# Performance work log

Measured on AMD Instinct MI355X. Metric: run time of the kernel, lower is better.

Reference implementation:

```python
import jax, jax.numpy as jnp
import numpy as np

S, B, D = 2048, 2, 4096
H, KVH, HD = 32, 8, 128          # n_heads_q, n_kv_heads, head_dim
NREP = H // KVH                  # GQA repeat factor
ROPE_BASE = 10000.0


def _rope(x, cos, sin):
    # x: [B, S, h, HD]; cos/sin: [S, HD//2]
    xr = x.reshape(x.shape[:-1] + (-1, 2))
    x0, x1 = xr[..., 0], xr[..., 1]
    c = cos[None, :, None, :]
    s = sin[None, :, None, :]
    out = jnp.stack([x0 * c - x1 * s, x0 * s + x1 * c], axis=-1)
    return out.reshape(x.shape)


def setup_inputs() -> dict:
    key = jax.random.key(0)
    k0, k1, k2, k3, k4 = jax.random.split(key, 5)
    x = jax.random.normal(k0, (S, B, D), jnp.float32)
    inv_freq = 1.0 / (ROPE_BASE ** (np.arange(0, HD, 2, dtype=np.float64) / HD))  # [HD//2]
    t = np.arange(S, dtype=np.float64)[:, None] * inv_freq[None, :]               # [S, HD//2]
    freqs_cos = jnp.asarray(np.cos(t), jnp.float32)
    freqs_sin = jnp.asarray(np.sin(t), jnp.float32)
    scale = 0.02
    wq = jax.random.normal(k1, (H * HD, D), jnp.float32) * scale
    wk = jax.random.normal(k2, (KVH * HD, D), jnp.float32) * scale
    wv = jax.random.normal(k3, (KVH * HD, D), jnp.float32) * scale
    wo = jax.random.normal(k4, (D, H * HD), jnp.float32) * scale
    return {"x": x, "start_pos": 0, "freqs_cos": freqs_cos, "freqs_sin": freqs_sin,
            "wq": wq, "wk": wk, "wv": wv, "wo": wo}


def reference(x, start_pos, freqs_cos, freqs_sin, wq, wk, wv, wo):
    seq_len, batch, _ = x.shape
    # QKV projections (torch Linear: y = x @ W^T), then [S,B,*] -> [B,S,h,HD]
    q = (x @ wq.T).transpose(1, 0, 2).reshape(batch, seq_len, H, HD)
    k = (x @ wk.T).transpose(1, 0, 2).reshape(batch, seq_len, KVH, HD)
    v = (x @ wv.T).transpose(1, 0, 2).reshape(batch, seq_len, KVH, HD)
    # RoPE on q and k
    q = _rope(q, freqs_cos, freqs_sin)
    k = _rope(k, freqs_cos, freqs_sin)
    # repeat_kv (GQA)
    k = jnp.repeat(k, NREP, axis=2)
    v = jnp.repeat(v, NREP, axis=2)
    # [B, H, S, HD]
    q = q.transpose(0, 2, 1, 3)
    k = k.transpose(0, 2, 1, 3)
    v = v.transpose(0, 2, 1, 3)
    # causal scaled dot-product attention (SDPA is_causal=True equivalent)
    scores = jnp.einsum('bhqd,bhkd->bhqk', q, k) / np.float32(np.sqrt(HD))
    causal = jnp.tril(jnp.ones((seq_len, seq_len), dtype=bool))
    scores = jnp.where(causal[None, None], scores, jnp.float32(-jnp.inf))
    probs = jax.nn.softmax(scores.astype(jnp.float32), axis=-1).astype(q.dtype)
    out = jnp.einsum('bhqk,bhkd->bhqd', probs, v)
    # [B,H,S,HD] -> [B,S,H*HD] -> [S,B,H*HD]
    out = out.transpose(0, 2, 1, 3).reshape(batch, seq_len, H * HD).transpose(1, 0, 2)
    return out @ wo.T
```

## Files before the change

kernel.cpp:

```cpp
#include <hip/hip_runtime.h>

typedef __attribute__((ext_vector_type(8))) short s16x8;
typedef __attribute__((ext_vector_type(8))) __bf16 bf16x8;
typedef __attribute__((ext_vector_type(4))) float f32x4;

#define S_LEN 2048
#define KDIM  4096
#define CSOFT 0.12751743f

__device__ __forceinline__ unsigned short f2bf(float f) {
  unsigned u = __builtin_bit_cast(unsigned, f);
  u += 0x7fffu + ((u >> 16) & 1u);
  return (unsigned short)(u >> 16);
}

__device__ __forceinline__ f32x4 mfma_bf16(s16x8 a, s16x8 b, f32x4 c) {
  return __builtin_amdgcn_mfma_f32_16x16x32_bf16(
      __builtin_bit_cast(bf16x8, a), __builtin_bit_cast(bf16x8, b), c, 0, 0, 0);
}

__device__ __forceinline__ void gload_lds16(const unsigned short* g, void* l) {
  __builtin_amdgcn_global_load_lds(
      (const __attribute__((address_space(1))) void*)g,
      (__attribute__((address_space(3))) void*)l, 16, 0, 0);
}

__global__ void cvt_bf16(const float* __restrict__ in,
                         unsigned short* __restrict__ out, int n8) {
  int i = blockIdx.x * 256 + threadIdx.x;
  if (i >= n8) return;
  const float* p = in + (size_t)i * 8;
  f32x4 a = *(const f32x4*)(p);
  f32x4 b = *(const f32x4*)(p + 4);
  s16x8 v;
  v[0] = (short)f2bf(a[0]); v[1] = (short)f2bf(a[1]);
  v[2] = (short)f2bf(a[2]); v[3] = (short)f2bf(a[3]);
  v[4] = (short)f2bf(b[0]); v[5] = (short)f2bf(b[1]);
  v[6] = (short)f2bf(b[2]); v[7] = (short)f2bf(b[3]);
  *(s16x8*)(out + (size_t)i * 8) = v;
}

template <int EPI, int N, bool B_FP32>
__global__ __launch_bounds__(256, 2)
void gemm_bt(const unsigned short* __restrict__ A,
             const float* __restrict__ Bw32,
             const unsigned short* __restrict__ Bw16,
             void* __restrict__ Out,
             const float* __restrict__ cosT,
             const float* __restrict__ sinT) {
  const int K = KDIM;
  const int tid = threadIdx.x;
  const int lane = tid & 63, wid = tid >> 6;
  const int l15 = lane & 15, l4 = lane >> 4;
  const int nct = N / 128;
  const int ct = blockIdx.x % nct, rt = blockIdx.x / nct;
  const int row0 = rt * 128, col0 = ct * 128;
  const int wr = wid >> 1, wc = wid & 1;

  __shared__ __align__(16) unsigned short As[128 * 32];
  __shared__ __align__(16) unsigned short Bs[128 * 32];

  f32x4 acc[4][4];
#pragma unroll
  for (int i = 0; i < 4; i++)
#pragma unroll
    for (int j = 0; j < 4; j++) acc[i][j] = f32x4{0.f, 0.f, 0.f, 0.f};

  for (int kt = 0; kt < K; kt += 32) {
#pragma unroll
    for (int i = 0; i < 2; i++) {
      int j = wid * 2 + i;
      int ch = j * 64 + lane;
      int r = ch >> 2, c = ch & 3;
      int sc = c ^ ((r >> 1) & 3);
      gload_lds16(A + (size_t)(row0 + r) * K + kt + sc * 8, (char*)As + j * 1024);
    }
    if (B_FP32) {
#pragma unroll
      for (int j = 0; j < 2; j++) {
        int ch = tid + 256 * j;
        int r = ch >> 2, c = ch & 3;
        const float* src = Bw32 + (size_t)(col0 + r) * K + kt + c * 8;
        f32x4 f0 = *(const f32x4*)(src);
        f32x4 f1 = *(const f32x4*)(src + 4);
        s16x8 v;
        v[0] = (short)f2bf(f0[0]); v[1] = (short)f2bf(f0[1]);
        v[2] = (short)f2bf(f0[2]); v[3] = (short)f2bf(f0[3]);
        v[4] = (short)f2bf(f1[0]); v[5] = (short)f2bf(f1[1]);
        v[6] = (short)f2bf(f1[2]); v[7] = (short)f2bf(f1[3]);
        int sw = c ^ ((r >> 1) & 3);
        *(s16x8*)((char*)Bs + r * 64 + sw * 16) = v;
      }
    } else {
#pragma unroll
      for (int i = 0; i < 2; i++) {
        int j = wid * 2 + i;
        int ch = j * 64 + lane;
        int r = ch >> 2, c = ch & 3;
        int sc = c ^ ((r >> 1) & 3);
        gload_lds16(Bw16 + (size_t)(col0 + r) * K + kt + sc * 8, (char*)Bs + j * 1024);
      }
    }
    __syncthreads();

    s16x8 af[4], bfr[4];
#pragma unroll
    for (int mi = 0; mi < 4; mi++) {
      int r = wr * 64 + mi * 16 + l15;
      int sw = l4 ^ ((r >> 1) & 3);
      af[mi] = *(const s16x8*)((char*)As + r * 64 + sw * 16);
    }
#pragma unroll
    for (int ni = 0; ni < 4; ni++) {
      int r = wc * 64 + ni * 16 + l15;
      int sw = l4 ^ ((r >> 1) & 3);
      bfr[ni] = *(const s16x8*)((char*)Bs + r * 64 + sw * 16);
    }
#pragma unroll
    for (int mi = 0; mi < 4; mi++)
#pragma unroll
      for (int ni = 0; ni < 4; ni++)
        acc[mi][ni] = mfma_bf16(af[mi], bfr[ni], acc[mi][ni]);
    __syncthreads();
  }

#pragma unroll
  for (int mi = 0; mi < 4; mi++) {
#pragma unroll
    for (int ni = 0; ni < 4; ni++) {
      f32x4 v = acc[mi][ni];
      int rowb = row0 + wr * 64 + mi * 16 + l4 * 4;
      int col = col0 + wc * 64 + ni * 16 + l15;
      if (EPI == 3) {
        float* o = (float*)Out;
#pragma unroll
        for (int r = 0; r < 4; r++) o[(size_t)(rowb + r) * 4096 + col] = v[r];
      } else {
        if (EPI != 2) {
          float vp[4];
#pragma unroll
          for (int r = 0; r < 4; r++) vp[r] = __shfl_xor(v[r], 1, 64);
          bool odd = lane & 1;
          int fi = (col & 127) >> 1;
#pragma unroll
          for (int r = 0; r < 4; r++) {
            int n = rowb + r, s = n >> 1;
            float c = cosT[s * 64 + fi], sn = sinT[s * 64 + fi];
            v[r] = odd ? (vp[r] * sn + v[r] * c) : (v[r] * c - vp[r] * sn);
          }
        }
        unsigned short* o = (unsigned short*)Out;
        int hh = col >> 7, hd = col & 127;
#pragma unroll
        for (int r = 0; r < 4; r++) {
          int n = rowb + r, s = n >> 1, b = n & 1;
          size_t idx;
          if (EPI == 0)      idx = ((size_t)(b * 32 + hh) * 2048 + s) * 128 + hd;
          else if (EPI == 1) idx = ((size_t)(b * 8 + hh) * 2048 + s) * 128 + hd;
          else               idx = ((size_t)(b * 8 + hh) * 128 + hd) * 2048 + s;
          o[idx] = f2bf(v[r]);
        }
      }
    }
  }
}

__global__ __launch_bounds__(256, 2)
void attn_fwd(const unsigned short* __restrict__ Qa,
              const unsigned short* __restrict__ Ka,
              const unsigned short* __restrict__ Vt,
              unsigned short* __restrict__ AO) {
  int bid = blockIdx.x;
  int pid = bid & 7;
  int h = (bid >> 3) & 31;
  int b = bid >> 8;
  int kvh = h >> 2;
  int tid = threadIdx.x, lane = tid & 63, wid = tid >> 6;
  int l15 = lane & 15, l4 = lane >> 4;

  __shared__ __align__(16) unsigned short Ks[64 * 128];
  __shared__ __align__(16) unsigned short Vs[128 * 64];
  __shared__ __align__(16) unsigned short Ps[4][32 * 64];

  const unsigned short* Qp = Qa + ((size_t)(b * 32 + h) * 2048) * 128;
  const unsigned short* Kp = Ka + ((size_t)(b * 8 + kvh) * 2048) * 128;
  const unsigned short* Vp = Vt + ((size_t)(b * 8 + kvh) * 128) * 2048;

  for (int half = 0; half < 2; half++) {
    int qt = half == 0 ? (7 - pid) : (8 + pid);
    int q0 = qt * 128, qr0 = q0 + wid * 32;

    s16x8 qf[2][4];
#pragma unroll
    for (int mi = 0; mi < 2; mi++)
#pragma unroll
      for (int ks = 0; ks < 4; ks++)
        qf[mi][ks] = *(const s16x8*)(Qp + (size_t)(qr0 + mi * 16 + l15) * 128 +
                                     ks * 32 + l4 * 8);

    f32x4 o[2][8];
#pragma unroll
    for (int mi = 0; mi < 2; mi++)
#pragma unroll
      for (int nb = 0; nb < 8; nb++) o[mi][nb] = f32x4{0.f, 0.f, 0.f, 0.f};
    float m[2][4], lsum[2][4];
#pragma unroll
    for (int mi = 0; mi < 2; mi++)
#pragma unroll
      for (int pr = 0; pr < 4; pr++) { m[mi][pr] = -1e30f; lsum[mi][pr] = 0.f; }

    int nt = q0 / 64 + 2;
    for (int t = 0; t < nt; t++) {
      int s0 = t * 64;
      const unsigned short* ktp = Kp + (size_t)s0 * 128;
#pragma unroll
      for (int i = 0; i < 4; i++) {
        int j = wid * 4 + i;
        int ch = j * 64 + lane;
        {
          int r = ch >> 4, cl = ch & 15;
          int sc = (cl & 8) | ((cl ^ (r & 7)) & 7);
          gload_lds16(ktp + r * 128 + sc * 8, (char*)Ks + j * 1024);
        }
        {
          int r = ch >> 3, p = ch & 7;
          int sc = p ^ (r & 7);
          gload_lds16(Vp + (size_t)r * 2048 + s0 + sc * 8, (char*)Vs + j * 1024);
        }
      }
      __syncthreads();

      if (s0 <= qr0 + 31) {
        f32x4 sc[2][4];
#pragma unroll
        for (int mi = 0; mi < 2; mi++)
#pragma unroll
          for (int kb = 0; kb < 4; kb++) sc[mi][kb] = f32x4{0.f, 0.f, 0.f, 0.f};
#pragma unroll
        for (int kb = 0; kb < 4; kb++) {
          int r = kb * 16 + l15;
#pragma unroll
          for (int ks = 0; ks < 4; ks++) {
            int c = ks * 4 + l4;
            int sw = (c & 8) | ((c ^ (r & 7)) & 7);
            s16x8 kf = *(const s16x8*)((char*)Ks + r * 256 + sw * 16);
            sc[0][kb] = mfma_bf16(qf[0][ks], kf, sc[0][kb]);
            sc[1][kb] = mfma_bf16(qf[1][ks], kf, sc[1][kb]);
          }
        }
        bool needmask = (s0 + 63) > qr0;
#pragma unroll
        for (int mi = 0; mi < 2; mi++) {
          if (needmask) {
#pragma unroll
            for (int kb = 0; kb < 4; kb++) {
              int kg = s0 + kb * 16 + l15;
#pragma unroll
              for (int pr = 0; pr < 4; pr++) {
                int qg = qr0 + mi * 16 + l4 * 4 + pr;
                if (kg > qg) sc[mi][kb][pr] = -1e30f;
              }
            }
          }
          float rm[4];
#pragma unroll
          for (int pr = 0; pr < 4; pr++)
            rm[pr] = fmaxf(fmaxf(sc[mi][0][pr], sc[mi][1][pr]),
                           fmaxf(sc[mi][2][pr], sc[mi][3][pr]));
#pragma unroll
          for (int xm = 1; xm <= 8; xm <<= 1)
#pragma unroll
            for (int pr = 0; pr < 4; pr++)
              rm[pr] = fmaxf(rm[pr], __shfl_xor(rm[pr], xm, 64));
          bool grow = false;
#pragma unroll
          for (int pr = 0; pr < 4; pr++)
            grow = grow || ((rm[pr] - m[mi][pr]) * CSOFT > 8.f);
          if (__any(grow)) {
            float fac[4];
#pragma unroll
            for (int pr = 0; pr < 4; pr++) {
              float nm = fmaxf(m[mi][pr], rm[pr]);
              fac[pr] = __builtin_amdgcn_exp2f((m[mi][pr] - nm) * CSOFT);
              m[mi][pr] = nm;
              lsum[mi][pr] *= fac[pr];
            }
#pragma unroll
            for (int nb = 0; nb < 8; nb++)
#pragma unroll
              for (int pr = 0; pr < 4; pr++) o[mi][nb][pr] *= fac[pr];
          }
          float rs[4] = {0.f, 0.f, 0.f, 0.f};
#pragma unroll
          for (int kb = 0; kb < 4; kb++)
#pragma unroll
            for (int pr = 0; pr < 4; pr++) {
              float p = __builtin_amdgcn_exp2f((sc[mi][kb][pr] - m[mi][pr]) * CSOFT);
              sc[mi][kb][pr] = p;
              rs[pr] += p;
            }
#pragma unroll
          for (int xm = 1; xm <= 8; xm <<= 1)
#pragma unroll
            for (int pr = 0; pr < 4; pr++) rs[pr] += __shfl_xor(rs[pr], xm, 64);
#pragma unroll
          for (int pr = 0; pr < 4; pr++) lsum[mi][pr] += rs[pr];
          char* pb = (char*)(&Ps[wid][0]);
#pragma unroll
          for (int kb = 0; kb < 4; kb++) {
            int col = kb * 16 + l15;
#pragma unroll
            for (int pr = 0; pr < 4; pr++) {
              int row = mi * 16 + l4 * 4 + pr;
              *(unsigned short*)(pb + row * 128 + (((col >> 3) ^ (row & 7)) * 16) +
                                 (col & 7) * 2) = f2bf(sc[mi][kb][pr]);
            }
          }
        }
        char* pb = (char*)(&Ps[wid][0]);
#pragma unroll
        for (int ks = 0; ks < 2; ks++) {
          s16x8 pa[2];
#pragma unroll
          for (int mi = 0; mi < 2; mi++) {
            int row = mi * 16 + l15;
            int c = ks * 4 + l4;
            pa[mi] = *(const s16x8*)(pb + row * 128 + ((c ^ (row & 7)) * 16));
          }
#pragma unroll
          for (int nb = 0; nb < 8; nb++) {
            int r = nb * 16 + l15;
            int c = ks * 4 + l4;
            s16x8 vf = *(const s16x8*)((char*)Vs + r * 128 + ((c ^ (r & 7)) * 16));
            o[0][nb] = mfma_bf16(pa[0], vf, o[0][nb]);
            o[1][nb] = mfma_bf16(pa[1], vf, o[1][nb]);
          }
        }
      }
      __syncthreads();
    }

#pragma unroll
    for (int mi = 0; mi < 2; mi++) {
      float inv[4];
#pragma unroll
      for (int pr = 0; pr < 4; pr++) inv[pr] = 1.f / lsum[mi][pr];
#pragma unroll
      for (int nb = 0; nb < 8; nb++) {
        int col = h * 128 + nb * 16 + l15;
#pragma unroll
        for (int pr = 0; pr < 4; pr++) {
          int q = qr0 + mi * 16 + l4 * 4 + pr;
          AO[(size_t)(q * 2 + b) * 4096 + col] = f2bf(o[mi][nb][pr] * inv[pr]);
        }
      }
    }
  }
}

extern "C" void kernel_launch(void* const* d_in, const int* in_sizes, int n_in,
                              void* d_out, int out_size, void* d_ws, size_t ws_size,
                              hipStream_t stream) {
  const float* x = (const float*)d_in[0];
  const float* cosT = (const float*)d_in[2];
  const float* sinT = (const float*)d_in[3];
  const float* wq = (const float*)d_in[4];
  const float* wk = (const float*)d_in[5];
  const float* wv = (const float*)d_in[6];
  const float* wo = (const float*)d_in[7];
  float* out = (float*)d_out;

  char* ws = (char*)d_ws;
  unsigned short* xb = (unsigned short*)(ws);
  unsigned short* Qa = (unsigned short*)(ws + 33554432ull);
  unsigned short* Ka = (unsigned short*)(ws + 67108864ull);
  unsigned short* Vt = (unsigned short*)(ws + 75497472ull);
  unsigned short* AO = (unsigned short*)(ws + 83886080ull);
  unsigned short* wqb = (unsigned short*)(ws + 117440512ull);
  unsigned short* wkb = (unsigned short*)(ws + 150994944ull);
  unsigned short* wvb = (unsigned short*)(ws + 159383552ull);
  unsigned short* wob = (unsigned short*)(ws + 167772160ull);
  bool wcvt = ws_size >= 201326592ull;

  cvt_bf16<<<8192, 256, 0, stream>>>(x, xb, 2097152);
  if (wcvt) {
    cvt_bf16<<<8192, 256, 0, stream>>>(wq, wqb, 2097152);
    cvt_bf16<<<2048, 256, 0, stream>>>(wk, wkb, 524288);
    cvt_bf16<<<2048, 256, 0, stream>>>(wv, wvb, 524288);
    cvt_bf16<<<8192, 256, 0, stream>>>(wo, wob, 2097152);
    gemm_bt<0, 4096, false><<<1024, 256, 0, stream>>>(xb, nullptr, wqb, Qa, cosT, sinT);
    gemm_bt<1, 1024, false><<<256, 256, 0, stream>>>(xb, nullptr, wkb, Ka, cosT, sinT);
    gemm_bt<2, 1024, false><<<256, 256, 0, stream>>>(xb, nullptr, wvb, Vt, cosT, sinT);
  } else {
    gemm_bt<0, 4096, true><<<1024, 256, 0, stream>>>(xb, wq, nullptr, Qa, cosT, sinT);
    gemm_bt<1, 1024, true><<<256, 256, 0, stream>>>(xb, wk, nullptr, Ka, cosT, sinT);
    gemm_bt<2, 1024, true><<<256, 256, 0, stream>>>(xb, wv, nullptr, Vt, cosT, sinT);
  }
  attn_fwd<<<512, 256, 0, stream>>>(Qa, Ka, Vt, AO);
  if (wcvt) {
    gemm_bt<3, 4096, false><<<1024, 256, 0, stream>>>(AO, nullptr, wob, out, cosT, sinT);
  } else {
    gemm_bt<3, 4096, true><<<1024, 256, 0, stream>>>(AO, wo, nullptr, out, cosT, sinT);
  }
}
```

Baseline: 670.3 us.

## Add 256x256-tile bf16 GEMM with staged async LDS prefetch for Q and O projections

Adds a gemm256 kernel using 256x256 output tiles with 8 waves. It double-buffers LDS through direct global-to-LDS loads, interleaved with MFMA phases, and uses XOR-swizzled LDS addressing, s_setprio and a remapped block order for L2 locality. The Q projection (with its fused RoPE epilogue) and the output projection move to this kernel; the K and V projections keep the old 128-tile GEMM. The larger tiles aim to raise arithmetic intensity and hide load latency. In exchange, the grid shrinks to 256 blocks with heavy register pressure, and the many barriers per k-step can stall waves.

```diff
diff --git a/kernel.cpp b/kernel.cpp
--- a/kernel.cpp
+++ b/kernel.cpp
@@ -38,6 +38,171 @@
   v[4] = (short)f2bf(b[0]); v[5] = (short)f2bf(b[1]);
   v[6] = (short)f2bf(b[2]); v[7] = (short)f2bf(b[3]);
   *(s16x8*)(out + (size_t)i * 8) = v;
+}
+
+template <int EPI>
+__global__ __launch_bounds__(512, 2)
+void gemm256(const unsigned short* __restrict__ A,
+             const unsigned short* __restrict__ B,
+             void* __restrict__ Out,
+             const float* __restrict__ cosT,
+             const float* __restrict__ sinT) {
+  const int K = KDIM;
+  const int NT = KDIM / 32;
+  __shared__ __align__(16) unsigned short As[2][256 * 32];
+  __shared__ __align__(16) unsigned short Bs[2][256 * 32];
+
+  const int tid = threadIdx.x;
+  const int lane = tid & 63, wid = tid >> 6;
+  const int l15 = lane & 15, l4 = lane >> 4;
+  const int wc = wid;
+
+  int bid = blockIdx.x;
+  int wg = (bid & 7) * 32 + (bid >> 3);
+  const int rt = wg >> 4, ct = wg & 15;
+  const int row0 = rt * 256, col0 = ct * 256;
+
+  {}
+  const int ch = wid * 64 + lane;
+  const int sL = ch >> 3, ss = ch & 7;
+  const int su = ss ^ (sL & 7);
+  const int sr = 2 * sL + (su >> 2);
+  const int sc = (su & 3) * 8;
+  const unsigned short* Asrc = A + (size_t)(row0 + sr) * K + sc;
+  const unsigned short* Bsrc = B + (size_t)(col0 + sr) * K + sc;
+
+  const int rdoff = (l15 >> 1) * 128 +
+                    (((((l15 & 1) << 2) | l4) ^ ((l15 >> 1) & 7)) << 4);
+
+  f32x4 acc[16][2];
+#pragma unroll
+  for (int i = 0; i < 16; i++) {
+    acc[i][0] = f32x4{0.f, 0.f, 0.f, 0.f};
+    acc[i][1] = f32x4{0.f, 0.f, 0.f, 0.f};
+  }
+
+  auto stage = [&](int buf, int half, bool isB, int kt) {
+    const unsigned short* src =
+        (isB ? Bsrc : Asrc) + (size_t)half * 128 * K + kt;
+    char* dst = (char*)(isB ? &Bs[buf][0] : &As[buf][0]) + half * 8192 +
+                wid * 1024;
+    gload_lds16(src, dst);
+  };
+
+  stage(0, 0, true, 0);
+  stage(0, 1, true, 0);
+  stage(0, 0, false, 0);
+  stage(0, 1, false, 0);
+  asm volatile("s_waitcnt vmcnt(1)" ::: "memory");
+  __builtin_amdgcn_s_barrier();
+  __builtin_amdgcn_sched_barrier(0);
+
+  for (int t = 0; t < NT; ++t) {
+    const int cur = t & 1, nxt = cur ^ 1;
+    const int ktn = (t + 1) * 32;
+    const bool pf = (t + 1) < NT;
+    const char* Ab = (const char*)&As[cur][0];
+    const char* Bb = (const char*)&Bs[cur][0];
+
+    s16x8 bf0 = *(const s16x8*)(Bb + wc * 2048 + rdoff);
+    s16x8 bf1 = *(const s16x8*)(Bb + wc * 2048 + 1024 + rdoff);
+    s16x8 afA[8];
+#pragma unroll
+    for (int mi = 0; mi < 8; mi++)
+      afA[mi] = *(const s16x8*)(Ab + mi * 1024 + rdoff);
+    if (pf) stage(nxt, 0, true, ktn);
+    __builtin_amdgcn_s_barrier();
+    __builtin_amdgcn_sched_barrier(0);
+    __builtin_amdgcn_s_setprio(1);
+#pragma unroll
+    for (int mi = 0; mi < 4; mi++) {
+      acc[mi][0] = mfma_bf16(afA[mi], bf0, acc[mi][0]);
+      acc[mi][1] = mfma_bf16(afA[mi], bf1, acc[mi][1]);
+    }
+    __builtin_amdgcn_s_setprio(0);
+    if (pf) { asm volatile("s_waitcnt vmcnt(1)" ::: "memory"); }
+    else    { asm volatile("s_waitcnt vmcnt(0)" ::: "memory"); }
+    __builtin_amdgcn_s_barrier();
+    __builtin_amdgcn_sched_barrier(0);
+
+    s16x8 afB[8];
+#pragma unroll
+    for (int mi = 0; mi < 8; mi++)
+      afB[mi] = *(const s16x8*)(Ab + 8192 + mi * 1024 + rdoff);
+    if (pf) stage(nxt, 1, true, ktn);
+    __builtin_amdgcn_s_barrier();
+    __builtin_amdgcn_sched_barrier(0);
+    __builtin_amdgcn_s_setprio(1);
+#pragma unroll
+    for (int mi = 4; mi < 8; mi++) {
+      acc[mi][0] = mfma_bf16(afA[mi], bf0, acc[mi][0]);
+      acc[mi][1] = mfma_bf16(afA[mi], bf1, acc[mi][1]);
+    }
+    __builtin_amdgcn_s_setprio(0);
+    __builtin_amdgcn_s_barrier();
+    __builtin_amdgcn_sched_barrier(0);
+
+    if (pf) stage(nxt, 0, false, ktn);
+    __builtin_amdgcn_s_barrier();
+    __builtin_amdgcn_sched_barrier(0);
+    __builtin_amdgcn_s_setprio(1);
+#pragma unroll
+    for (int mi = 0; mi < 4; mi++) {
+      acc[8 + mi][0] = mfma_bf16(afB[mi], bf0, acc[8 + mi][0]);
+      acc[8 + mi][1] = mfma_bf16(afB[mi], bf1, acc[8 + mi][1]);
+    }
+    __builtin_amdgcn_s_setprio(0);
+    __builtin_amdgcn_s_barrier();
+    __builtin_amdgcn_sched_barrier(0);
+
+    if (pf) stage(nxt, 1, false, ktn);
+    __builtin_amdgcn_s_barrier();
+    __builtin_amdgcn_sched_barrier(0);
+    __builtin_amdgcn_s_setprio(1);
+#pragma unroll
+    for (int mi = 4; mi < 8; mi++) {
+      acc[8 + mi][0] = mfma_bf16(afB[mi], bf0, acc[8 + mi][0]);
+      acc[8 + mi][1] = mfma_bf16(afB[mi], bf1, acc[8 + mi][1]);
+    }
+    __builtin_amdgcn_s_setprio(0);
+    if (pf) { asm volatile("s_waitcnt vmcnt(1)" ::: "memory"); }
+    __builtin_amdgcn_s_barrier();
+    __builtin_amdgcn_sched_barrier(0);
+  }
+
+#pragma unroll
+  for (int mi = 0; mi < 16; mi++) {
+#pragma unroll
+    for (int ni = 0; ni < 2; ni++) {
+      f32x4 v = acc[mi][ni];
+      int rowb = row0 + mi * 16 + l4 * 4;
+      int col = col0 + wc * 32 + ni * 16 + l15;
+      if (EPI == 3) {
+        float* o = (float*)Out;
+#pragma unroll
+        for (int r = 0; r < 4; r++) o[(size_t)(rowb + r) * 4096 + col] = v[r];
+      } else {
+        float vp[4];
+#pragma unroll
+        for (int r = 0; r < 4; r++) vp[r] = __shfl_xor(v[r], 1, 64);
+        bool odd = lane & 1;
+        int fi = (col & 127) >> 1;
+#pragma unroll
+        for (int r = 0; r < 4; r++) {
+          int n = rowb + r, s = n >> 1;
+          float c = cosT[s * 64 + fi], sn = sinT[s * 64 + fi];
+          v[r] = odd ? (vp[r] * sn + v[r] * c) : (v[r] * c - vp[r] * sn);
+        }
+        unsigned short* o = (unsigned short*)Out;
+        int hh = col >> 7, hd = col & 127;
+#pragma unroll
+        for (int r = 0; r < 4; r++) {
+          int n = rowb + r, s = n >> 1, b = n & 1;
+          o[((size_t)(b * 32 + hh) * 2048 + s) * 128 + hd] = f2bf(v[r]);
+        }
+      }
+    }
+  }
 }
 
 template <int EPI, int N, bool B_FP32>
@@ -388,7 +553,7 @@
     cvt_bf16<<<2048, 256, 0, stream>>>(wk, wkb, 524288);
     cvt_bf16<<<2048, 256, 0, stream>>>(wv, wvb, 524288);
     cvt_bf16<<<8192, 256, 0, stream>>>(wo, wob, 2097152);
-    gemm_bt<0, 4096, false><<<1024, 256, 0, stream>>>(xb, nullptr, wqb, Qa, cosT, sinT);
+    gemm256<0><<<256, 512, 0, stream>>>(xb, wqb, Qa, cosT, sinT);
     gemm_bt<1, 1024, false><<<256, 256, 0, stream>>>(xb, nullptr, wkb, Ka, cosT, sinT);
     gemm_bt<2, 1024, false><<<256, 256, 0, stream>>>(xb, nullptr, wvb, Vt, cosT, sinT);
   } else {
@@ -398,7 +563,7 @@
   }
   attn_fwd<<<512, 256, 0, stream>>>(Qa, Ka, Vt, AO);
   if (wcvt) {
-    gemm_bt<3, 4096, false><<<1024, 256, 0, stream>>>(AO, nullptr, wob, out, cosT, sinT);
+    gemm256<3><<<256, 512, 0, stream>>>(AO, wob, out, cosT, sinT);
   } else {
     gemm_bt<3, 4096, true><<<1024, 256, 0, stream>>>(AO, wo, nullptr, out, cosT, sinT);
   }
```

New measurement: 640.9 us. 4.4% less time.

## Add 256x256-tile 8-wave GEMM with interleaved LDS staging for Q and O projections

Applied to the files above, without the earlier changes.

Introduces a new GEMM kernel with 256x256 output tiles, 512 threads, double-buffered LDS staged via global_load_lds, XOR-swizzled LDS layout, sub-phase interleaving of loads and MFMAs with setprio, and an XCD-aware block remap. It replaces the 128x128 GEMM for the Q projection (with RoPE epilogue) and the output projection when bf16 weights are available. Larger tiles halve global traffic per FLOP. The cost is one block per CU with heavy register use, and only 256 blocks, which may underfill a GPU with 256 CUs.

```diff
diff --git a/kernel.cpp b/kernel.cpp
--- a/kernel.cpp
+++ b/kernel.cpp
@@ -38,6 +38,194 @@
   v[4] = (short)f2bf(b[0]); v[5] = (short)f2bf(b[1]);
   v[6] = (short)f2bf(b[2]); v[7] = (short)f2bf(b[3]);
   *(s16x8*)(out + (size_t)i * 8) = v;
+}
+
+template <int EPI>
+__global__ __launch_bounds__(512, 1)
+void gemm256(const unsigned short* __restrict__ A,
+             const unsigned short* __restrict__ B,
+             void* __restrict__ Out,
+             const float* __restrict__ cosT,
+             const float* __restrict__ sinT) {
+  const int K = KDIM;
+  __shared__ __align__(16) unsigned short As[2 * 2 * 8192];
+  __shared__ __align__(16) unsigned short Bs[2 * 2 * 8192];
+
+  const int tid = threadIdx.x;
+  const int lane = tid & 63, wid = tid >> 6;
+  const int l15 = lane & 15, l4 = lane >> 4;
+  const int wr = wid >> 2, wc = wid & 3;
+
+  int bid = blockIdx.x;
+  int wg = (bid & 7) * 32 + (bid >> 3);
+  const int rt = wg >> 4, ct = wg & 15;
+  const int row0 = rt * 256, col0 = ct * 256;
+
+  const int ch0 = tid, ch1 = 512 + tid;
+  const int sr0 = ch0 >> 3, u0 = (ch0 & 7) ^ (sr0 & 7);
+  const int sr1 = ch1 >> 3, u1 = (ch1 & 7) ^ (sr1 & 7);
+  const unsigned short* A0p = A + (size_t)(row0 + sr0) * K + u0 * 8;
+  const unsigned short* A1p = A + (size_t)(row0 + sr1) * K + u1 * 8;
+  const unsigned short* B0p = B + (size_t)(col0 + sr0) * K + u0 * 8;
+  const unsigned short* B1p = B + (size_t)(col0 + sr1) * K + u1 * 8;
+
+  const int rdo0 = l15 * 128 + ((l4 ^ (l15 & 7)) << 4);
+  const int rdo1 = l15 * 128 + (((4 | l4) ^ (l15 & 7)) << 4);
+
+  f32x4 acc[8][4];
+#pragma unroll
+  for (int m = 0; m < 8; m++)
+#pragma unroll
+    for (int n = 0; n < 4; n++) acc[m][n] = f32x4{0.f, 0.f, 0.f, 0.f};
+
+  auto stageA = [&](int buf, int h, int kt) {
+    char* d = (char*)As + buf * 32768 + h * 16384 + wid * 1024;
+    size_t so = (size_t)h * 128 * K + kt;
+    gload_lds16(A0p + so, d);
+    gload_lds16(A1p + so, d + 8192);
+  };
+  auto stageB = [&](int buf, int h, int kt) {
+    char* d = (char*)Bs + buf * 32768 + h * 16384 + wid * 1024;
+    size_t so = (size_t)h * 128 * K + kt;
+    gload_lds16(B0p + so, d);
+    gload_lds16(B1p + so, d + 8192);
+  };
+  auto barsb = [&]() {
+    __builtin_amdgcn_s_barrier();
+    __builtin_amdgcn_sched_barrier(0);
+  };
+
+  stageA(0, 0, 0);
+  stageA(0, 1, 0);
+  stageB(0, 0, 0);
+  stageB(0, 1, 0);
+  stageA(1, 0, 64);
+  asm volatile("s_waitcnt vmcnt(2)" ::: "memory");
+  barsb();
+
+  auto do_tile = [&](int tau, bool s123, bool s4, int vmend) {
+    const int buf = tau & 1;
+    const char* Ab = (const char*)As + buf * 32768 + wr * 16384;
+    const char* Bb = (const char*)Bs + buf * 32768 + (wc >> 1) * 16384 +
+                     (wc & 1) * 8192;
+    const int kt1 = (tau + 1) * 64, kt2 = (tau + 2) * 64;
+    s16x8 af0[4], af1[4], bA0[2], bA1[2], bB0[2], bB1[2];
+
+#pragma unroll
+    for (int mi = 0; mi < 4; mi++) {
+      af0[mi] = *(const s16x8*)(Ab + mi * 2048 + rdo0);
+      af1[mi] = *(const s16x8*)(Ab + mi * 2048 + rdo1);
+    }
+#pragma unroll
+    for (int ni = 0; ni < 2; ni++) {
+      bA0[ni] = *(const s16x8*)(Bb + ni * 2048 + rdo0);
+      bA1[ni] = *(const s16x8*)(Bb + ni * 2048 + rdo1);
+    }
+    if (s123) stageA(buf ^ 1, 1, kt1);
+    barsb();
+    __builtin_amdgcn_s_setprio(1);
+#pragma unroll
+    for (int mi = 0; mi < 4; mi++)
+#pragma unroll
+      for (int ni = 0; ni < 2; ni++) {
+        acc[mi][ni] = mfma_bf16(af0[mi], bA0[ni], acc[mi][ni]);
+        acc[mi][ni] = mfma_bf16(af1[mi], bA1[ni], acc[mi][ni]);
+      }
+    __builtin_amdgcn_s_setprio(0);
+    barsb();
+
+#pragma unroll
+    for (int ni = 0; ni < 2; ni++) {
+      bB0[ni] = *(const s16x8*)(Bb + (2 + ni) * 2048 + rdo0);
+      bB1[ni] = *(const s16x8*)(Bb + (2 + ni) * 2048 + rdo1);
+    }
+    if (s123) stageB(buf ^ 1, 0, kt1);
+    barsb();
+    __builtin_amdgcn_s_setprio(1);
+#pragma unroll
+    for (int mi = 0; mi < 4; mi++)
+#pragma unroll
+      for (int ni = 0; ni < 2; ni++) {
+        acc[mi][2 + ni] = mfma_bf16(af0[mi], bB0[ni], acc[mi][2 + ni]);
+        acc[mi][2 + ni] = mfma_bf16(af1[mi], bB1[ni], acc[mi][2 + ni]);
+      }
+    __builtin_amdgcn_s_setprio(0);
+    barsb();
+
+#pragma unroll
+    for (int mi = 0; mi < 4; mi++) {
+      af0[mi] = *(const s16x8*)(Ab + 8192 + mi * 2048 + rdo0);
+      af1[mi] = *(const s16x8*)(Ab + 8192 + mi * 2048 + rdo1);
+    }
+    if (s123) stageB(buf ^ 1, 1, kt1);
+    barsb();
+    __builtin_amdgcn_s_setprio(1);
+#pragma unroll
+    for (int mi = 0; mi < 4; mi++)
+#pragma unroll
+      for (int ni = 0; ni < 2; ni++) {
+        acc[4 + mi][2 + ni] = mfma_bf16(af0[mi], bB0[ni], acc[4 + mi][2 + ni]);
+        acc[4 + mi][2 + ni] = mfma_bf16(af1[mi], bB1[ni], acc[4 + mi][2 + ni]);
+      }
+    __builtin_amdgcn_s_setprio(0);
+    barsb();
+
+    if (s4) stageA(buf, 0, kt2);
+    barsb();
+    __builtin_amdgcn_s_setprio(1);
+#pragma unroll
+    for (int mi = 0; mi < 4; mi++)
+#pragma unroll
+      for (int ni = 0; ni < 2; ni++) {
+        acc[4 + mi][ni] = mfma_bf16(af0[mi], bA0[ni], acc[4 + mi][ni]);
+        acc[4 + mi][ni] = mfma_bf16(af1[mi], bA1[ni], acc[4 + mi][ni]);
+      }
+    __builtin_amdgcn_s_setprio(0);
+    if (vmend == 2) {
+      asm volatile("s_waitcnt vmcnt(2)" ::: "memory");
+    } else if (vmend == 0) {
+      asm volatile("s_waitcnt vmcnt(0)" ::: "memory");
+    }
+    barsb();
+  };
+
+  for (int tau = 0; tau < 62; tau++) do_tile(tau, true, true, 2);
+  do_tile(62, true, false, 0);
+  do_tile(63, false, false, -1);
+
+#pragma unroll
+  for (int m = 0; m < 8; m++) {
+#pragma unroll
+    for (int n = 0; n < 4; n++) {
+      f32x4 v = acc[m][n];
+      int rowb = row0 + wr * 128 + m * 16 + l4 * 4;
+      int col = col0 + wc * 64 + n * 16 + l15;
+      if (EPI == 3) {
+        float* o = (float*)Out;
+#pragma unroll
+        for (int r = 0; r < 4; r++) o[(size_t)(rowb + r) * 4096 + col] = v[r];
+      } else {
+        float vp[4];
+#pragma unroll
+        for (int r = 0; r < 4; r++) vp[r] = __shfl_xor(v[r], 1, 64);
+        bool odd = lane & 1;
+        int fi = (col & 127) >> 1;
+#pragma unroll
+        for (int r = 0; r < 4; r++) {
+          int nn = rowb + r, s = nn >> 1;
+          float c = cosT[s * 64 + fi], sn = sinT[s * 64 + fi];
+          v[r] = odd ? (vp[r] * sn + v[r] * c) : (v[r] * c - vp[r] * sn);
+        }
+        unsigned short* o = (unsigned short*)Out;
+        int hh = col >> 7, hd = col & 127;
+#pragma unroll
+        for (int r = 0; r < 4; r++) {
+          int nn = rowb + r, s = nn >> 1, b = nn & 1;
+          o[((size_t)(b * 32 + hh) * 2048 + s) * 128 + hd] = f2bf(v[r]);
+        }
+      }
+    }
+  }
 }
 
 template <int EPI, int N, bool B_FP32>
@@ -388,7 +576,7 @@
     cvt_bf16<<<2048, 256, 0, stream>>>(wk, wkb, 524288);
     cvt_bf16<<<2048, 256, 0, stream>>>(wv, wvb, 524288);
     cvt_bf16<<<8192, 256, 0, stream>>>(wo, wob, 2097152);
-    gemm_bt<0, 4096, false><<<1024, 256, 0, stream>>>(xb, nullptr, wqb, Qa, cosT, sinT);
+    gemm256<0><<<256, 512, 0, stream>>>(xb, wqb, Qa, cosT, sinT);
     gemm_bt<1, 1024, false><<<256, 256, 0, stream>>>(xb, nullptr, wkb, Ka, cosT, sinT);
     gemm_bt<2, 1024, false><<<256, 256, 0, stream>>>(xb, nullptr, wvb, Vt, cosT, sinT);
   } else {
@@ -398,7 +586,7 @@
   }
   attn_fwd<<<512, 256, 0, stream>>>(Qa, Ka, Vt, AO);
   if (wcvt) {
-    gemm_bt<3, 4096, false><<<1024, 256, 0, stream>>>(AO, nullptr, wob, out, cosT, sinT);
+    gemm256<3><<<256, 512, 0, stream>>>(AO, wob, out, cosT, sinT);
   } else {
     gemm_bt<3, 4096, true><<<1024, 256, 0, stream>>>(AO, wo, nullptr, out, cosT, sinT);
   }
```

Measured after the change: 620.1 us. 7.5% less time.
